# Optimization experiments

Hardware: AMD Instinct MI355X
Metric: run time of the kernel (lower is better)

## Reference

```python
import jax, jax.numpy as jnp
import numpy as np

B, L, DIN, DH, DE = 16, 128, 768, 300, 100
ALPHA = 0.2
NEG = -9e15


def setup_inputs() -> dict:
    key = jax.random.key(0)
    k = jax.random.split(key, 7)
    s = lambda fan: 1.0 / np.sqrt(fan)
    return {
        "x": jax.random.normal(k[0], (B, L, DIN), jnp.float32),
        "adj": jax.random.randint(k[1], (B, L, L), 0, 2, jnp.int32),
        "edge_embedding": jax.random.normal(k[2], (B, L, L, DE), jnp.float32),
        "W": jax.random.normal(k[3], (DIN, DH), jnp.float32) * s(DIN),
        "a": jax.random.normal(k[4], (2 * DH, 1), jnp.float32) * s(2 * DH),
        "edge_map_w": jax.random.normal(k[5], (DH, DE), jnp.float32) * s(DE),
        "edge_map_b": jnp.zeros((DH,), jnp.float32),
        "edge_lin_w": jax.random.normal(k[6], (1, DH), jnp.float32) * s(DH),
        "edge_lin_b": jnp.zeros((1,), jnp.float32),
    }


def _forward(x, edge_embedding, W, a, edge_map_w, edge_map_b, edge_lin_w, edge_lin_b, adj):
    h = x @ W  # [B, L, DH]
    # Faithful to torch: h.repeat_interleave(L, dim=2).view(B, L*L, DH) scrambles
    # features: a_input_first[b, i*L+j, d] = h[b, i, (j*DH + d) // L].
    # So e1[b,i,j] = sum_d h[b,i,(j*DH+d)//L] * a[d] = h[b,i] . V[j], with V[j,k] =
    # sum of a[d] over d where (j*DH+d)//L == k. Build V once by scatter-add.
    idx = (jnp.arange(L)[:, None] * DH + jnp.arange(DH)[None, :]) // L  # [L, DH], values in [0, DH)
    a_first = a[:DH, 0]
    V = jnp.zeros((L, DH), h.dtype).at[jnp.arange(L)[:, None], idx].add(a_first[None, :])  # [L, DH]
    e1 = jnp.einsum('bik,jk->bij', h, V)  # [B, L, L]
    # Second half: h.repeat_interleave(L, dim=0).view(...) gives plain h_j tiling.
    e2 = h @ a[DH:, 0]  # [B, L], broadcast over i
    e = jax.nn.leaky_relu(e1 + e2[:, None, :], ALPHA)  # [B, L, L]
    # Edge-weight gate (use_edge_weight == 'yes'); note torch relu result is discarded.
    em = edge_embedding @ edge_map_w.T + edge_map_b  # [B, L, L, DH]
    ew = jax.nn.sigmoid(em @ edge_lin_w.T + edge_lin_b)[..., 0]  # [B, L, L]
    e_final = e * ew
    att = jax.nn.softmax(jnp.where(adj > 0, e_final, NEG), axis=2)  # dropout off (eval)
    return h + jnp.matmul(att, h)  # residual add, concat=False


def reference(x, adj, edge_embedding, W, a, edge_map_w, edge_map_b, edge_lin_w, edge_lin_b):
    return _forward(x, edge_embedding, W, a, edge_map_w, edge_map_b, edge_lin_w, edge_lin_b, adj)
```

## Files before the change

### kernel.cpp

```cpp
#include <hip/hip_runtime.h>
#include <hip/hip_bf16.h>


#define L 128
#define DH 300
#define DIN 768
#define DE 100
#define SPLITK 4
#define MROWS 2048
#define IG 2
#define SL ((size_t)MROWS * DH)

typedef __bf16 bf16x8 __attribute__((ext_vector_type(8)));
typedef float f32x4 __attribute__((ext_vector_type(4)));
typedef unsigned short ushort_t;

__device__ __forceinline__ ushort_t f2bf(float f) {
    __bf16 h = (__bf16)f;
    ushort_t u;
    __builtin_memcpy(&u, &h, 2);
    return u;
}

__global__ __launch_bounds__(256) void k_small(
    const float* __restrict__ A,
    const float* __restrict__ EMW,
    const float* __restrict__ EMB,
    const float* __restrict__ ELW,
    const float* __restrict__ ELB,
    float* __restrict__ CV, float* __restrict__ C0,
    float* __restrict__ VW, int* __restrict__ VCOL)
{
    int t = threadIdx.x;
    if (blockIdx.x == 0) {
        if (t < DE) {
            float s = 0.f;
            for (int k = 0; k < DH; ++k)
                s += ELW[k] * EMW[k * DE + t];
            CV[t] = s;
        } else if (t == DE) {
            float s = 0.f;
            for (int k = 0; k < DH; ++k)
                s += ELW[k] * EMB[k];
            C0[0] = s + ELB[0];
        }
    } else {
        if (t < L) {
            int base = t * DH;
            int cm = base >> 7;
            float w0 = 0.f, w1 = 0.f, w2 = 0.f, w3 = 0.f;
            for (int j = 0; j < DH; ++j) {
                int u = ((base + j) >> 7) - cm;
                float av = A[j];
                w0 += (u == 0) ? av : 0.f;
                w1 += (u == 1) ? av : 0.f;
                w2 += (u == 2) ? av : 0.f;
                w3 += (u == 3) ? av : 0.f;
            }
            VCOL[t] = cm;
            VW[t * 4 + 0] = w0; VW[t * 4 + 1] = w1;
            VW[t * 4 + 2] = w2; VW[t * 4 + 3] = w3;
        }
    }
}

__global__ __launch_bounds__(256) void k_cvt(
    const float* __restrict__ Wm, ushort_t* __restrict__ WT)
{
    __shared__ float tile[64][65];
    int k0 = blockIdx.x * 64;
    int c0 = blockIdx.y * 64;
    int t = threadIdx.x;
#pragma unroll
    for (int s = 0; s < 16; ++s) {
        int idx = t + 256 * s;
        int kr = idx >> 6, cc = idx & 63;
        int c = c0 + cc;
        tile[kr][cc] = (c < DH) ? Wm[(size_t)(k0 + kr) * DH + c] : 0.f;
    }
    __syncthreads();
#pragma unroll
    for (int s = 0; s < 16; ++s) {
        int idx = t + 256 * s;
        int c = idx >> 6, kr = idx & 63;
        WT[(size_t)(c0 + c) * DIN + k0 + kr] = f2bf(tile[kr][c]);
    }
}

__global__ __launch_bounds__(256) void k_gemm(
    const float* __restrict__ X,
    const ushort_t* __restrict__ WT,
    float* __restrict__ HP)
{
    __shared__ ushort_t As[64 * 72];
    __shared__ ushort_t Bs[64 * 72];
    int t = threadIdx.x;
    int w = t >> 6;
    int lane = t & 63;
    int lr = lane & 15;
    int lk = lane >> 4;
    int r0 = blockIdx.y * 64;
    int c0 = blockIdx.x * 64;
    int kbase = blockIdx.z * (DIN / SPLITK);

    f32x4 acc[4];
#pragma unroll
    for (int ct = 0; ct < 4; ++ct) acc[ct] = (f32x4){0.f, 0.f, 0.f, 0.f};

    int srow = t >> 2, skq = (t & 3) * 16;

    for (int step = 0; step < 3; ++step) {
        int kk = kbase + step * 64;
        {
            const float4* xs = (const float4*)(X + (size_t)(r0 + srow) * DIN + kk + skq);
            float4 f0 = xs[0], f1 = xs[1], f2 = xs[2], f3 = xs[3];
            bf16x8 v0, v1;
            v0[0] = (__bf16)f0.x; v0[1] = (__bf16)f0.y; v0[2] = (__bf16)f0.z; v0[3] = (__bf16)f0.w;
            v0[4] = (__bf16)f1.x; v0[5] = (__bf16)f1.y; v0[6] = (__bf16)f1.z; v0[7] = (__bf16)f1.w;
            v1[0] = (__bf16)f2.x; v1[1] = (__bf16)f2.y; v1[2] = (__bf16)f2.z; v1[3] = (__bf16)f2.w;
            v1[4] = (__bf16)f3.x; v1[5] = (__bf16)f3.y; v1[6] = (__bf16)f3.z; v1[7] = (__bf16)f3.w;
            *(bf16x8*)&As[srow * 72 + skq] = v0;
            *(bf16x8*)&As[srow * 72 + skq + 8] = v1;
        }
        {
            const uint4* wp = (const uint4*)(WT + (size_t)(c0 + srow) * DIN + kk + skq);
            uint4 u0 = wp[0], u1 = wp[1];
            *(uint4*)&Bs[srow * 72 + skq] = u0;
            *(uint4*)&Bs[srow * 72 + skq + 8] = u1;
        }
        __syncthreads();
#pragma unroll
        for (int k2 = 0; k2 < 2; ++k2) {
            bf16x8 af = *(bf16x8*)&As[(w * 16 + lr) * 72 + k2 * 32 + lk * 8];
#pragma unroll
            for (int ct = 0; ct < 4; ++ct) {
                bf16x8 bf_ = *(bf16x8*)&Bs[(ct * 16 + lr) * 72 + k2 * 32 + lk * 8];
                acc[ct] = __builtin_amdgcn_mfma_f32_16x16x32_bf16(af, bf_, acc[ct], 0, 0, 0);
            }
        }
        __syncthreads();
    }
    float* outp = HP + (size_t)blockIdx.z * SL;
#pragma unroll
    for (int ct = 0; ct < 4; ++ct) {
        int col = c0 + ct * 16 + lr;
        if (col < DH) {
#pragma unroll
            for (int r = 0; r < 4; ++r) {
                int row = r0 + w * 16 + lk * 4 + r;
                outp[(size_t)row * DH + col] = acc[ct][r];
            }
        }
    }
}

__global__ __launch_bounds__(256) void k_red(
    const float* __restrict__ HP, const float* __restrict__ A,
    float* __restrict__ H, float* __restrict__ E2)
{
    int t = threadIdx.x;
    int row = blockIdx.x * 8 + (t >> 5);
    int lane = t & 31;
    const float4* a4 = (const float4*)(A + DH);
    float4* hout = (float4*)(H + (size_t)row * DH);
    float acc = 0.f;
    for (int k4 = lane; k4 < DH / 4; k4 += 32) {
        float4 hv; hv.x = 0.f; hv.y = 0.f; hv.z = 0.f; hv.w = 0.f;
#pragma unroll
        for (int z = 0; z < SPLITK; ++z) {
            float4 v = ((const float4*)(HP + (size_t)z * SL + (size_t)row * DH))[k4];
            hv.x += v.x; hv.y += v.y; hv.z += v.z; hv.w += v.w;
        }
        float4 av = a4[k4];
        hout[k4] = hv;
        acc += hv.x * av.x + hv.y * av.y + hv.z * av.z + hv.w * av.w;
    }
#pragma unroll
    for (int o = 16; o >= 1; o >>= 1) acc += __shfl_xor(acc, o);
    if (lane == 0) E2[row] = acc;
}

__global__ __launch_bounds__(256) void k_ef(
    const float* __restrict__ EE, const float* __restrict__ CV,
    const float* __restrict__ C0, float* __restrict__ S)
{
    __shared__ float eeb[32 * DE];
    __shared__ float cl[DE];
    int bid = blockIdx.x;
    int t = threadIdx.x;
    if (t < DE) cl[t] = CV[t];
    int jg = t >> 3;
    int g  = t & 7;
    const float c0v = C0[0];
#pragma unroll
    for (int ch = 0; ch < 4; ++ch) {
        __syncthreads();
        const float4* src = (const float4*)(EE + (size_t)bid * (L * DE) + ch * 32 * DE);
        float4* dst = (float4*)eeb;
        for (int idx = t; idx < 800; idx += 256) dst[idx] = src[idx];
        __syncthreads();
        const float2* row = (const float2*)(eeb + jg * DE);
        const float2* cp = (const float2*)cl;
        float s = 0.f;
        for (int q = g; q < 50; q += 8) {
            float2 v = row[q], c2 = cp[q];
            s = fmaf(v.x, c2.x, fmaf(v.y, c2.y, s));
        }
        s += __shfl_xor(s, 1);
        s += __shfl_xor(s, 2);
        s += __shfl_xor(s, 4);
        if (g == 0) S[(size_t)bid * L + ch * 32 + jg] = s + c0v;
    }
}

__global__ __launch_bounds__(256) void k_sm_pv(
    const float* __restrict__ S, const int* __restrict__ ADJ,
    const float* __restrict__ H, const float* __restrict__ E2,
    const float* __restrict__ VW, const int* __restrict__ VCOL,
    float* __restrict__ OUT)
{
    __shared__ float hrow[IG][DH];
    __shared__ float att[IG][L];
    int blk = blockIdx.x;
    int b = blk >> 6;
    int i0 = (blk & 63) * IG;
    int bid0 = b * L + i0;
    int t = threadIdx.x;

    for (int idx = t; idx < IG * DH; idx += 256) {
        int r = idx / DH, k = idx - r * DH;
        hrow[r][k] = H[(size_t)(bid0 + r) * DH + k];
    }
    __syncthreads();

    {
        int r = t >> 7, j = t & 127;
        int bid = bid0 + r;
        float s = S[(size_t)bid * L + j];
        float ewv = 1.f / (1.f + expf(-s));
        int cm = VCOL[j];
        float e1 = 0.f;
#pragma unroll
        for (int u = 0; u < 4; ++u) {
            int c = cm + u; if (c > DH - 1) c = DH - 1;
            e1 += VW[j * 4 + u] * hrow[r][c];
        }
        float e = e1 + E2[(size_t)b * L + j];
        e = (e > 0.f) ? e : 0.2f * e;
        att[r][j] = (ADJ[(size_t)bid * L + j] > 0) ? e * ewv : -9.0e15f;
    }
    __syncthreads();

    {
        int w = t >> 6, lane = t & 63;
        if (w < IG) {
            float v0 = att[w][lane], v1 = att[w][lane + 64];
            float m = fmaxf(v0, v1);
#pragma unroll
            for (int o = 32; o >= 1; o >>= 1) m = fmaxf(m, __shfl_xor(m, o));
            float p0 = expf(v0 - m), p1 = expf(v1 - m);
            float sm = p0 + p1;
#pragma unroll
            for (int o = 32; o >= 1; o >>= 1) sm += __shfl_xor(sm, o);
            float inv = 1.f / sm;
            att[w][lane] = p0 * inv;
            att[w][lane + 64] = p1 * inv;
        }
    }
    __syncthreads();

    const float* Hb = H + (size_t)b * L * DH;
    for (int k = t; k < DH; k += 256) {
        float a0 = hrow[0][k], c0a = 0.f;
        float a1 = hrow[1][k], c1a = 0.f;
#pragma unroll 2
        for (int j = 0; j < L; j += 4) {
            float h0 = Hb[(size_t)(j + 0) * DH + k];
            float h1 = Hb[(size_t)(j + 1) * DH + k];
            float h2 = Hb[(size_t)(j + 2) * DH + k];
            float h3 = Hb[(size_t)(j + 3) * DH + k];
            a0  = fmaf(att[0][j + 0], h0, a0);
            c0a = fmaf(att[0][j + 1], h1, c0a);
            a0  = fmaf(att[0][j + 2], h2, a0);
            c0a = fmaf(att[0][j + 3], h3, c0a);
            a1  = fmaf(att[1][j + 0], h0, a1);
            c1a = fmaf(att[1][j + 1], h1, c1a);
            a1  = fmaf(att[1][j + 2], h2, a1);
            c1a = fmaf(att[1][j + 3], h3, c1a);
        }
        OUT[(size_t)(bid0 + 0) * DH + k] = a0 + c0a;
        OUT[(size_t)(bid0 + 1) * DH + k] = a1 + c1a;
    }
}

extern "C" void kernel_launch(void* const* d_in, const int* in_sizes, int n_in,
                              void* d_out, int out_size, void* d_ws, size_t ws_size,
                              hipStream_t stream) {
    const float* X   = (const float*)d_in[0];
    const int*   ADJ = (const int*)d_in[1];
    const float* EE  = (const float*)d_in[2];
    const float* Wm  = (const float*)d_in[3];
    const float* A   = (const float*)d_in[4];
    const float* EMW = (const float*)d_in[5];
    const float* EMB = (const float*)d_in[6];
    const float* ELW = (const float*)d_in[7];
    const float* ELB = (const float*)d_in[8];
    float* OUT = (float*)d_out;

    float* ws = (float*)d_ws;
    float* HP   = ws;
    float* H    = ws + 2457600;
    float* E2   = ws + 3072000;
    float* CV   = ws + 3074048;
    float* C0   = ws + 3074148;
    float* VW   = ws + 3074152;
    int*   VCOL = (int*)(ws + 3074664);
    ushort_t* WT = (ushort_t*)(ws + 3074816);
    float* Sbuf = ws + 3197696;

    k_small<<<dim3(2), dim3(256), 0, stream>>>(A, EMW, EMB, ELW, ELB, CV, C0, VW, VCOL);
    k_cvt<<<dim3(12, 5), dim3(256), 0, stream>>>(Wm, WT);
    k_gemm<<<dim3(5, 32, SPLITK), dim3(256), 0, stream>>>(X, WT, HP);
    k_red<<<dim3(256), dim3(256), 0, stream>>>(HP, A, H, E2);
    k_ef<<<dim3(2048), dim3(256), 0, stream>>>(EE, CV, C0, Sbuf);
    k_sm_pv<<<dim3(1024), dim3(256), 0, stream>>>(Sbuf, ADJ, H, E2, VW, VCOL, OUT);
}
```

Before: 72.34 us.

## Load edge-embedding block into registers up front and reduce partial dot products via LDS

The edge-gate kernel used to stage the 128x100 edge-embedding slab through shared memory in four chunks, with two barriers per chunk and a strided per-row dot product. Now each thread issues all 13 float4 global loads at once into registers, multiplies each float4 by the matching 4-wide slice of the gate vector, and writes that partial sum to shared memory. Pairs of threads then each sum about half of a row's 25 partials and combine them with a shuffle. The goal is more memory loads in flight and fewer barriers on this bandwidth-bound pass, at the cost of higher register use and strided shared-memory reads that may cause bank conflicts.

```diff
diff --git a/kernel.cpp b/kernel.cpp
--- a/kernel.cpp
+++ b/kernel.cpp
@@ -184,33 +184,41 @@
     const float* __restrict__ EE, const float* __restrict__ CV,
     const float* __restrict__ C0, float* __restrict__ S)
 {
-    __shared__ float eeb[32 * DE];
-    __shared__ float cl[DE];
+    __shared__ __align__(16) float cl[DE];
+    __shared__ float ps[3200];
     int bid = blockIdx.x;
     int t = threadIdx.x;
+    const float4* src = (const float4*)(EE + (size_t)bid * (L * DE));
+
+    float4 v[13];
+#pragma unroll
+    for (int s = 0; s < 12; ++s) v[s] = src[t + 256 * s];
+    if (t < 128) v[12] = src[t + 3072];
+    else { v[12].x = 0.f; v[12].y = 0.f; v[12].z = 0.f; v[12].w = 0.f; }
+
     if (t < DE) cl[t] = CV[t];
-    int jg = t >> 3;
-    int g  = t & 7;
-    const float c0v = C0[0];
-#pragma unroll
-    for (int ch = 0; ch < 4; ++ch) {
-        __syncthreads();
-        const float4* src = (const float4*)(EE + (size_t)bid * (L * DE) + ch * 32 * DE);
-        float4* dst = (float4*)eeb;
-        for (int idx = t; idx < 800; idx += 256) dst[idx] = src[idx];
-        __syncthreads();
-        const float2* row = (const float2*)(eeb + jg * DE);
-        const float2* cp = (const float2*)cl;
-        float s = 0.f;
-        for (int q = g; q < 50; q += 8) {
-            float2 v = row[q], c2 = cp[q];
-            s = fmaf(v.x, c2.x, fmaf(v.y, c2.y, s));
-        }
-        s += __shfl_xor(s, 1);
-        s += __shfl_xor(s, 2);
-        s += __shfl_xor(s, 4);
-        if (g == 0) S[(size_t)bid * L + ch * 32 + jg] = s + c0v;
-    }
+    __syncthreads();
+
+    int p = t % 25;
+#pragma unroll
+    for (int s = 0; s < 13; ++s) {
+        int idx = t + 256 * s;
+        if (s < 12 || t < 128) {
+            float4 c4 = *(const float4*)&cl[p * 4];
+            ps[idx] = v[s].x * c4.x + v[s].y * c4.y + v[s].z * c4.z + v[s].w * c4.w;
+        }
+        p += 6; if (p >= 25) p -= 25;
+    }
+    __syncthreads();
+
+    int r = t >> 1, h = t & 1;
+    const float* pp = ps + 25 * r + h * 13;
+    float s0 = 0.f;
+#pragma unroll
+    for (int m = 0; m < 12; ++m) s0 += pp[m];
+    if (h == 0) s0 += pp[12];
+    s0 += __shfl_xor(s0, 1);
+    if (h == 0) S[(size_t)bid * L + r] = s0 + C0[0];
 }
 
 __global__ __launch_bounds__(256) void k_sm_pv(
```

After: 71.84 us. About the same (-0.7%).
